# Kernel tuning notes

Measured on AMD Instinct MI355X. Metric: run time of the kernel, lower is better.

## Reference

```python
import jax, jax.numpy as jnp
import numpy as np

EPS = 1e-12

def _l2norm(x):
    # F.normalize(x, p=2, dim=1) applied on [B*N, D] == normalize last dim of [B, N, D]
    return x / jnp.maximum(jnp.linalg.norm(x, axis=-1, keepdims=True), EPS)

def setup_inputs() -> dict:
    key = jax.random.key(0)
    k1, k2 = jax.random.split(key)
    B, N, D = 128, 64, 128  # batch_size, num_epoch, feature_dim
    feat_k = jax.random.normal(k1, (B, N, D), dtype=jnp.float32)
    feat_q = jax.random.normal(k2, (B, N, D), dtype=jnp.float32)
    return {"feat_k": feat_k, "feat_q": feat_q}

def reference(feat_k, feat_q):
    B, N, D = feat_k.shape
    fk = _l2norm(feat_k)                       # [B, N, D]
    fq = jax.lax.stop_gradient(_l2norm(feat_q))  # sampler branch is no_grad

    # Dense pairwise similarities, as in the original einsum('ijk,mnk->ijnm')
    logits = jnp.einsum('ijk,mnk->ijnm', fk, fk)  # [B, N, N, B]
    sim    = jnp.einsum('ijk,mnk->ijnm', fq, fq)  # [B, N, N, B]

    el = jnp.exp(logits)

    # mask[i, j, n, m] = (m == i):
    #   pos[i, j] = sum_n exp(logits[i, j, n, i])
    pos = jnp.einsum('ijni->ij', el)              # diagonal over (i, m), summed over n

    #   neg[i, j] = sum_{n, m != i} exp(logits[i, j, n, m]) * sim[i, j, n, m]
    prod = el * sim
    neg = prod.sum(axis=(2, 3)) - jnp.einsum('ijni->ij', prod)

    loss = jnp.mean(-jnp.log(pos / (pos + neg)))
    return loss
```

## Files before the change

### kernel.cpp

```cpp
#include <hip/hip_runtime.h>
#include <stdint.h>

#define ROWS 8192
#define D    128
#define CSPLIT 16
#define CPS  (ROWS / CSPLIT)
#define BM   256
#define BN   64
#define NT   (CPS / BN)

typedef __bf16 bf16x8 __attribute__((ext_vector_type(8)));
typedef float  f32x4  __attribute__((ext_vector_type(4)));

typedef const __attribute__((address_space(1))) uint32_t guint;
typedef __attribute__((address_space(3))) uint32_t luint;

__device__ __forceinline__ void gload_lds16(const void* g, void* l) {
    __builtin_amdgcn_global_load_lds((guint*)g, (luint*)l, 16, 0, 0);
}

__device__ __forceinline__ ushort f2bf(float f) {
    union { float f; uint32_t u; } x; x.f = f;
    uint32_t r = x.u + 0x7FFFu + ((x.u >> 16) & 1u);
    return (ushort)(r >> 16);
}

__global__ __launch_bounds__(256) void k_norm(
    const float* __restrict__ fk, const float* __restrict__ fq,
    ushort* __restrict__ fkn, ushort* __restrict__ fqn)
{
    int gw = (blockIdx.x * 256 + threadIdx.x) >> 6;
    int l  = threadIdx.x & 63;
    const float* src; ushort* dst; int r;
    if (gw < ROWS) { src = fk; dst = fkn; r = gw; }
    else           { src = fq; dst = fqn; r = gw - ROWS; }
    float2 v = *reinterpret_cast<const float2*>(&src[r * D + l * 2]);
    float ss = v.x * v.x + v.y * v.y;
    #pragma unroll
    for (int m = 1; m < 64; m <<= 1) ss += __shfl_xor(ss, m, 64);
    float inv = 1.0f / fmaxf(sqrtf(ss), 1e-12f);
    ushort2 o; o.x = f2bf(v.x * inv); o.y = f2bf(v.y * inv);
    *reinterpret_cast<ushort2*>(&dst[r * D + l * 2]) = o;
}

__global__ __launch_bounds__(512, 4) void k_gram(
    const ushort* __restrict__ fkn, const ushort* __restrict__ fqn,
    float* __restrict__ pneg, float* __restrict__ ppos)
{
    __shared__ ushort lds[2][2 * BN * D];
    const int rt = blockIdx.x;
    const int cs = blockIdx.y;
    const int w  = threadIdx.x >> 6;
    const int l  = threadIdx.x & 63;
    const int lrow = l >> 4, lcol = l & 15;
    const int r0 = rt * BM;

    int off[2];
    #pragma unroll
    for (int i = 0; i < 2; ++i) {
        int L = w * 128 + i * 64 + l;
        int row = L >> 4, slot = L & 15;
        int col = slot ^ (row & 7);
        off[i] = row * 256 + col * 16;
    }

    bf16x8 ak[2][4], aq[2][4];
    #pragma unroll
    for (int rg = 0; rg < 2; ++rg) {
        int arow = r0 + w * 32 + rg * 16 + lcol;
        #pragma unroll
        for (int ks = 0; ks < 4; ++ks) {
            ak[rg][ks] = *reinterpret_cast<const bf16x8*>(fkn + arow * D + ks * 32 + lrow * 8);
            aq[rg][ks] = *reinterpret_cast<const bf16x8*>(fqn + arow * D + ks * 32 + lrow * 8);
        }
    }

    const int diagc = ((r0 + w * 32) >> 6) << 6;

    auto issue_stage = [&](int buf, int cbase) {
        const char* fkb = (const char*)fkn + (size_t)cbase * 256;
        const char* fqb = (const char*)fqn + (size_t)cbase * 256;
        ushort* lk = &lds[buf][w * 1024];
        ushort* lq = &lds[buf][BN * D + w * 1024];
        gload_lds16(fkb + off[0], lk);
        gload_lds16(fkb + off[1], lk + 512);
        gload_lds16(fqb + off[0], lq);
        gload_lds16(fqb + off[1], lq + 512);
    };

    float accp[2][4] = {{0.f,0.f,0.f,0.f},{0.f,0.f,0.f,0.f}};
    float accn[2][4] = {{0.f,0.f,0.f,0.f},{0.f,0.f,0.f,0.f}};

    issue_stage(0, cs * CPS);
    __syncthreads();

    int cur = 0;
    for (int t = 0; t < NT; ++t) {
        const int cbase = cs * CPS + t * BN;
        if (t + 1 < NT) issue_stage(cur ^ 1, cbase + BN);
        const bool diag = (cbase == diagc);
        const ushort* bkb = &lds[cur][0];
        const ushort* bqb = &lds[cur][BN * D];
        #pragma unroll
        for (int cc = 0; cc < 4; ++cc) {
            int brow = cc * 16 + lcol;
            f32x4 sk0 = {0,0,0,0}, sk1 = {0,0,0,0}, sq0 = {0,0,0,0}, sq1 = {0,0,0,0};
            #pragma unroll
            for (int ks = 0; ks < 4; ++ks) {
                int slot = (ks * 4 + lrow) ^ (brow & 7);
                bf16x8 bk = *reinterpret_cast<const bf16x8*>(bkb + brow * D + slot * 8);
                bf16x8 bq = *reinterpret_cast<const bf16x8*>(bqb + brow * D + slot * 8);
                sk0 = __builtin_amdgcn_mfma_f32_16x16x32_bf16(ak[0][ks], bk, sk0, 0, 0, 0);
                sk1 = __builtin_amdgcn_mfma_f32_16x16x32_bf16(ak[1][ks], bk, sk1, 0, 0, 0);
                sq0 = __builtin_amdgcn_mfma_f32_16x16x32_bf16(aq[0][ks], bq, sq0, 0, 0, 0);
                sq1 = __builtin_amdgcn_mfma_f32_16x16x32_bf16(aq[1][ks], bq, sq1, 0, 0, 0);
            }
            if (diag) {
                #pragma unroll
                for (int e = 0; e < 4; ++e) {
                    accp[0][e] += __expf(sk0[e]);
                    accp[1][e] += __expf(sk1[e]);
                }
            } else {
                #pragma unroll
                for (int e = 0; e < 4; ++e) {
                    accn[0][e] += __expf(sk0[e]) * sq0[e];
                    accn[1][e] += __expf(sk1[e]) * sq1[e];
                }
            }
        }
        __syncthreads();
        cur ^= 1;
    }

    #pragma unroll
    for (int m = 1; m <= 8; m <<= 1) {
        #pragma unroll
        for (int rg = 0; rg < 2; ++rg)
            #pragma unroll
            for (int e = 0; e < 4; ++e) {
                accp[rg][e] += __shfl_xor(accp[rg][e], m, 64);
                accn[rg][e] += __shfl_xor(accn[rg][e], m, 64);
            }
    }
    if (lcol == 0) {
        #pragma unroll
        for (int rg = 0; rg < 2; ++rg)
            #pragma unroll
            for (int e = 0; e < 4; ++e) {
                int gr = r0 + w * 32 + rg * 16 + lrow * 4 + e;
                ppos[cs * ROWS + gr] = accp[rg][e];
                pneg[cs * ROWS + gr] = accn[rg][e];
            }
    }
}

__global__ __launch_bounds__(256) void k_loss1(
    const float* __restrict__ pneg, const float* __restrict__ ppos,
    float* __restrict__ bsum)
{
    int r = blockIdx.x * 256 + threadIdx.x;
    float pos = 0.f, neg = 0.f;
    #pragma unroll
    for (int p = 0; p < CSPLIT; ++p) { pos += ppos[p * ROWS + r]; neg += pneg[p * ROWS + r]; }
    float s = log1pf(neg / pos);
    #pragma unroll
    for (int m = 1; m < 64; m <<= 1) s += __shfl_xor(s, m, 64);
    __shared__ float red[4];
    if ((threadIdx.x & 63) == 0) red[threadIdx.x >> 6] = s;
    __syncthreads();
    if (threadIdx.x == 0) bsum[blockIdx.x] = red[0] + red[1] + red[2] + red[3];
}

__global__ void k_loss2(const float* __restrict__ bsum, float* __restrict__ out)
{
    int l = threadIdx.x;
    float s = (l < 32) ? bsum[l] : 0.f;
    #pragma unroll
    for (int m = 1; m < 64; m <<= 1) s += __shfl_xor(s, m, 64);
    if (l == 0) out[0] = s * (1.0f / ROWS);
}

extern "C" void kernel_launch(void* const* d_in, const int* in_sizes, int n_in,
                              void* d_out, int out_size, void* d_ws, size_t ws_size,
                              hipStream_t stream)
{
    const float* fk = (const float*)d_in[0];
    const float* fq = (const float*)d_in[1];
    ushort* fkn = (ushort*)d_ws;
    ushort* fqn = fkn + ROWS * D;
    float*  pneg = (float*)(fqn + ROWS * D);
    float*  ppos = pneg + CSPLIT * ROWS;
    float*  bsum = ppos + CSPLIT * ROWS;

    k_norm<<<(2 * ROWS) / 4, 256, 0, stream>>>(fk, fq, fkn, fqn);
    k_gram<<<dim3(ROWS / BM, CSPLIT), 512, 0, stream>>>(fkn, fqn, pneg, ppos);
    k_loss1<<<32, 256, 0, stream>>>(pneg, ppos, bsum);
    k_loss2<<<1, 64, 0, stream>>>(bsum, (float*)d_out);
}
```

Measured before the change: 51.20 us.

## Use 4 waves with 64 rows each, fold log2e into k-normalization

Halves the gram block to 4 waves, each owning 64 A rows (4 row groups), so every B fragment read from LDS feeds four MFMAs instead of two. This cuts LDS read traffic per MFMA, at the cost of more registers and fewer resident waves. It also pre-scales the normalized k features by sqrt(log2 e), so the Gram entries are already in log2 units and a raw exp2 can replace __expf. The first tile's async load is issued before the A fragments are loaded, to overlap the two.

```diff
diff --git a/kernel.cpp b/kernel.cpp
--- a/kernel.cpp
+++ b/kernel.cpp
@@ -8,6 +8,7 @@
 #define BM   256
 #define BN   64
 #define NT   (CPS / BN)
+#define SQRT_LOG2E 1.2011224087864498f
 
 typedef __bf16 bf16x8 __attribute__((ext_vector_type(8)));
 typedef float  f32x4  __attribute__((ext_vector_type(4)));
@@ -31,19 +32,19 @@
 {
     int gw = (blockIdx.x * 256 + threadIdx.x) >> 6;
     int l  = threadIdx.x & 63;
-    const float* src; ushort* dst; int r;
-    if (gw < ROWS) { src = fk; dst = fkn; r = gw; }
-    else           { src = fq; dst = fqn; r = gw - ROWS; }
+    const float* src; ushort* dst; int r; float scale;
+    if (gw < ROWS) { src = fk; dst = fkn; r = gw; scale = SQRT_LOG2E; }
+    else           { src = fq; dst = fqn; r = gw - ROWS; scale = 1.0f; }
     float2 v = *reinterpret_cast<const float2*>(&src[r * D + l * 2]);
     float ss = v.x * v.x + v.y * v.y;
     #pragma unroll
     for (int m = 1; m < 64; m <<= 1) ss += __shfl_xor(ss, m, 64);
-    float inv = 1.0f / fmaxf(sqrtf(ss), 1e-12f);
+    float inv = scale / fmaxf(sqrtf(ss), 1e-12f);
     ushort2 o; o.x = f2bf(v.x * inv); o.y = f2bf(v.y * inv);
     *reinterpret_cast<ushort2*>(&dst[r * D + l * 2]) = o;
 }
 
-__global__ __launch_bounds__(512, 4) void k_gram(
+__global__ __launch_bounds__(256, 2) void k_gram(
     const ushort* __restrict__ fkn, const ushort* __restrict__ fqn,
     float* __restrict__ pneg, float* __restrict__ ppos)
 {
@@ -55,19 +56,31 @@
     const int lrow = l >> 4, lcol = l & 15;
     const int r0 = rt * BM;
 
-    int off[2];
-    #pragma unroll
-    for (int i = 0; i < 2; ++i) {
-        int L = w * 128 + i * 64 + l;
+    int off[4];
+    #pragma unroll
+    for (int t = 0; t < 4; ++t) {
+        int L = t * 256 + w * 64 + l;
         int row = L >> 4, slot = L & 15;
         int col = slot ^ (row & 7);
-        off[i] = row * 256 + col * 16;
-    }
-
-    bf16x8 ak[2][4], aq[2][4];
-    #pragma unroll
-    for (int rg = 0; rg < 2; ++rg) {
-        int arow = r0 + w * 32 + rg * 16 + lcol;
+        off[t] = row * 256 + col * 16;
+    }
+
+    auto issue_stage = [&](int buf, int cbase) {
+        const char* fkb = (const char*)fkn + (size_t)cbase * 256;
+        const char* fqb = (const char*)fqn + (size_t)cbase * 256;
+        #pragma unroll
+        for (int t = 0; t < 4; ++t) {
+            gload_lds16(fkb + off[t], &lds[buf][t * 2048 + w * 512]);
+            gload_lds16(fqb + off[t], &lds[buf][BN * D + t * 2048 + w * 512]);
+        }
+    };
+
+    issue_stage(0, cs * CPS);
+
+    bf16x8 ak[4][4], aq[4][4];
+    #pragma unroll
+    for (int rg = 0; rg < 4; ++rg) {
+        int arow = r0 + w * 64 + rg * 16 + lcol;
         #pragma unroll
         for (int ks = 0; ks < 4; ++ks) {
             ak[rg][ks] = *reinterpret_cast<const bf16x8*>(fkn + arow * D + ks * 32 + lrow * 8);
@@ -75,23 +88,11 @@
         }
     }
 
-    const int diagc = ((r0 + w * 32) >> 6) << 6;
-
-    auto issue_stage = [&](int buf, int cbase) {
-        const char* fkb = (const char*)fkn + (size_t)cbase * 256;
-        const char* fqb = (const char*)fqn + (size_t)cbase * 256;
-        ushort* lk = &lds[buf][w * 1024];
-        ushort* lq = &lds[buf][BN * D + w * 1024];
-        gload_lds16(fkb + off[0], lk);
-        gload_lds16(fkb + off[1], lk + 512);
-        gload_lds16(fqb + off[0], lq);
-        gload_lds16(fqb + off[1], lq + 512);
-    };
-
-    float accp[2][4] = {{0.f,0.f,0.f,0.f},{0.f,0.f,0.f,0.f}};
-    float accn[2][4] = {{0.f,0.f,0.f,0.f},{0.f,0.f,0.f,0.f}};
-
-    issue_stage(0, cs * CPS);
+    const int diagc = r0 + w * 64;
+
+    float accp[4][4] = {};
+    float accn[4][4] = {};
+
     __syncthreads();
 
     int cur = 0;
@@ -104,29 +105,31 @@
         #pragma unroll
         for (int cc = 0; cc < 4; ++cc) {
             int brow = cc * 16 + lcol;
-            f32x4 sk0 = {0,0,0,0}, sk1 = {0,0,0,0}, sq0 = {0,0,0,0}, sq1 = {0,0,0,0};
+            f32x4 sk[4] = {{0,0,0,0},{0,0,0,0},{0,0,0,0},{0,0,0,0}};
+            f32x4 sq[4] = {{0,0,0,0},{0,0,0,0},{0,0,0,0},{0,0,0,0}};
             #pragma unroll
             for (int ks = 0; ks < 4; ++ks) {
                 int slot = (ks * 4 + lrow) ^ (brow & 7);
                 bf16x8 bk = *reinterpret_cast<const bf16x8*>(bkb + brow * D + slot * 8);
                 bf16x8 bq = *reinterpret_cast<const bf16x8*>(bqb + brow * D + slot * 8);
-                sk0 = __builtin_amdgcn_mfma_f32_16x16x32_bf16(ak[0][ks], bk, sk0, 0, 0, 0);
-                sk1 = __builtin_amdgcn_mfma_f32_16x16x32_bf16(ak[1][ks], bk, sk1, 0, 0, 0);
-                sq0 = __builtin_amdgcn_mfma_f32_16x16x32_bf16(aq[0][ks], bq, sq0, 0, 0, 0);
-                sq1 = __builtin_amdgcn_mfma_f32_16x16x32_bf16(aq[1][ks], bq, sq1, 0, 0, 0);
+                #pragma unroll
+                for (int rg = 0; rg < 4; ++rg) {
+                    sk[rg] = __builtin_amdgcn_mfma_f32_16x16x32_bf16(ak[rg][ks], bk, sk[rg], 0, 0, 0);
+                    sq[rg] = __builtin_amdgcn_mfma_f32_16x16x32_bf16(aq[rg][ks], bq, sq[rg], 0, 0, 0);
+                }
             }
             if (diag) {
                 #pragma unroll
-                for (int e = 0; e < 4; ++e) {
-                    accp[0][e] += __expf(sk0[e]);
-                    accp[1][e] += __expf(sk1[e]);
-                }
+                for (int rg = 0; rg < 4; ++rg)
+                    #pragma unroll
+                    for (int e = 0; e < 4; ++e)
+                        accp[rg][e] += __builtin_exp2f(sk[rg][e]);
             } else {
                 #pragma unroll
-                for (int e = 0; e < 4; ++e) {
-                    accn[0][e] += __expf(sk0[e]) * sq0[e];
-                    accn[1][e] += __expf(sk1[e]) * sq1[e];
-                }
+                for (int rg = 0; rg < 4; ++rg)
+                    #pragma unroll
+                    for (int e = 0; e < 4; ++e)
+                        accn[rg][e] += __builtin_exp2f(sk[rg][e]) * sq[rg][e];
             }
         }
         __syncthreads();
@@ -136,7 +139,7 @@
     #pragma unroll
     for (int m = 1; m <= 8; m <<= 1) {
         #pragma unroll
-        for (int rg = 0; rg < 2; ++rg)
+        for (int rg = 0; rg < 4; ++rg)
             #pragma unroll
             for (int e = 0; e < 4; ++e) {
                 accp[rg][e] += __shfl_xor(accp[rg][e], m, 64);
@@ -145,10 +148,10 @@
     }
     if (lcol == 0) {
         #pragma unroll
-        for (int rg = 0; rg < 2; ++rg)
+        for (int rg = 0; rg < 4; ++rg)
             #pragma unroll
             for (int e = 0; e < 4; ++e) {
-                int gr = r0 + w * 32 + rg * 16 + lrow * 4 + e;
+                int gr = r0 + w * 64 + rg * 16 + lrow * 4 + e;
                 ppos[cs * ROWS + gr] = accp[rg][e];
                 pneg[cs * ROWS + gr] = accn[rg][e];
             }
@@ -194,7 +197,7 @@
     float*  bsum = ppos + CSPLIT * ROWS;
 
     k_norm<<<(2 * ROWS) / 4, 256, 0, stream>>>(fk, fq, fkn, fqn);
-    k_gram<<<dim3(ROWS / BM, CSPLIT), 512, 0, stream>>>(fkn, fqn, pneg, ppos);
+    k_gram<<<dim3(ROWS / BM, CSPLIT), 256, 0, stream>>>(fkn, fqn, pneg, ppos);
     k_loss1<<<32, 256, 0, stream>>>(pneg, ppos, bsum);
     k_loss2<<<1, 64, 0, stream>>>(bsum, (float*)d_out);
 }
```

Measured after the change: 55.90 us. +9.2%, slower.

## Deepen LDS pipeline to four stages and fold log2e into normalization

Applied to the files above, without the earlier changes.

Reworks the gram kernel's staging from a double buffer of 64-column tiles to a four-deep ring of 32-column tiles. Three stages are prefetched up front and the loop waits with a manual vmcnt wait and a single barrier. The k vectors are prescaled by sqrt(log2 e) so exp2 can replace expf, B fragments are loaded before the MFMA chain, and setprio is raised around the MFMAs. The aim is to hide global-to-LDS latency and trim exp cost, at the price of more barriers per column and some fragile hand-written wait counts.

```diff
diff --git a/kernel.cpp b/kernel.cpp
--- a/kernel.cpp
+++ b/kernel.cpp
@@ -6,8 +6,9 @@
 #define CSPLIT 16
 #define CPS  (ROWS / CSPLIT)
 #define BM   256
-#define BN   64
+#define BN   32
 #define NT   (CPS / BN)
+#define SQRT_LOG2E 1.2011224087864498f
 
 typedef __bf16 bf16x8 __attribute__((ext_vector_type(8)));
 typedef float  f32x4  __attribute__((ext_vector_type(4)));
@@ -31,14 +32,14 @@
 {
     int gw = (blockIdx.x * 256 + threadIdx.x) >> 6;
     int l  = threadIdx.x & 63;
-    const float* src; ushort* dst; int r;
-    if (gw < ROWS) { src = fk; dst = fkn; r = gw; }
-    else           { src = fq; dst = fqn; r = gw - ROWS; }
+    const float* src; ushort* dst; int r; float scale;
+    if (gw < ROWS) { src = fk; dst = fkn; r = gw; scale = SQRT_LOG2E; }
+    else           { src = fq; dst = fqn; r = gw - ROWS; scale = 1.0f; }
     float2 v = *reinterpret_cast<const float2*>(&src[r * D + l * 2]);
     float ss = v.x * v.x + v.y * v.y;
     #pragma unroll
     for (int m = 1; m < 64; m <<= 1) ss += __shfl_xor(ss, m, 64);
-    float inv = 1.0f / fmaxf(sqrtf(ss), 1e-12f);
+    float inv = scale / fmaxf(sqrtf(ss), 1e-12f);
     ushort2 o; o.x = f2bf(v.x * inv); o.y = f2bf(v.y * inv);
     *reinterpret_cast<ushort2*>(&dst[r * D + l * 2]) = o;
 }
@@ -47,7 +48,7 @@
     const ushort* __restrict__ fkn, const ushort* __restrict__ fqn,
     float* __restrict__ pneg, float* __restrict__ ppos)
 {
-    __shared__ ushort lds[2][2 * BN * D];
+    __shared__ ushort lds[4][2][BN][128];
     const int rt = blockIdx.x;
     const int cs = blockIdx.y;
     const int w  = threadIdx.x >> 6;
@@ -55,14 +56,22 @@
     const int lrow = l >> 4, lcol = l & 15;
     const int r0 = rt * BM;
 
-    int off[2];
-    #pragma unroll
-    for (int i = 0; i < 2; ++i) {
-        int L = w * 128 + i * 64 + l;
+    int soff;
+    {
+        int L = threadIdx.x;
         int row = L >> 4, slot = L & 15;
-        int col = slot ^ (row & 7);
-        off[i] = row * 256 + col * 16;
-    }
+        soff = row * 256 + (slot ^ (row & 7)) * 16;
+    }
+
+    auto issue_stage = [&](int buf, int cbase) {
+        gload_lds16((const char*)fkn + (size_t)cbase * 256 + soff, &lds[buf][0][0][0] + (size_t)threadIdx.x * 8);
+        gload_lds16((const char*)fqn + (size_t)cbase * 256 + soff, &lds[buf][1][0][0] + (size_t)threadIdx.x * 8);
+    };
+
+    const int cbase0 = cs * CPS;
+    issue_stage(0, cbase0);
+    issue_stage(1, cbase0 + BN);
+    issue_stage(2, cbase0 + 2 * BN);
 
     bf16x8 ak[2][4], aq[2][4];
     #pragma unroll
@@ -75,62 +84,54 @@
         }
     }
 
-    const int diagc = ((r0 + w * 32) >> 6) << 6;
-
-    auto issue_stage = [&](int buf, int cbase) {
-        const char* fkb = (const char*)fkn + (size_t)cbase * 256;
-        const char* fqb = (const char*)fqn + (size_t)cbase * 256;
-        ushort* lk = &lds[buf][w * 1024];
-        ushort* lq = &lds[buf][BN * D + w * 1024];
-        gload_lds16(fkb + off[0], lk);
-        gload_lds16(fkb + off[1], lk + 512);
-        gload_lds16(fqb + off[0], lq);
-        gload_lds16(fqb + off[1], lq + 512);
-    };
-
-    float accp[2][4] = {{0.f,0.f,0.f,0.f},{0.f,0.f,0.f,0.f}};
-    float accn[2][4] = {{0.f,0.f,0.f,0.f},{0.f,0.f,0.f,0.f}};
-
-    issue_stage(0, cs * CPS);
-    __syncthreads();
-
-    int cur = 0;
+    const int diagc = (r0 + w * 32) & ~63;
+
+    float accp[2][4] = {};
+    float accn[2][4] = {};
+
     for (int t = 0; t < NT; ++t) {
-        const int cbase = cs * CPS + t * BN;
-        if (t + 1 < NT) issue_stage(cur ^ 1, cbase + BN);
-        const bool diag = (cbase == diagc);
-        const ushort* bkb = &lds[cur][0];
-        const ushort* bqb = &lds[cur][BN * D];
-        #pragma unroll
-        for (int cc = 0; cc < 4; ++cc) {
+        asm volatile("s_waitcnt vmcnt(4)" ::: "memory");
+        __builtin_amdgcn_s_barrier();
+        if (t + 3 < NT) issue_stage((t + 3) & 3, cbase0 + (t + 3) * BN);
+
+        const int cbase = cbase0 + t * BN;
+        const bool diag = ((cbase & ~63) == diagc);
+        const ushort* bkb = &lds[t & 3][0][0][0];
+        const ushort* bqb = &lds[t & 3][1][0][0];
+        #pragma unroll
+        for (int cc = 0; cc < 2; ++cc) {
             int brow = cc * 16 + lcol;
-            f32x4 sk0 = {0,0,0,0}, sk1 = {0,0,0,0}, sq0 = {0,0,0,0}, sq1 = {0,0,0,0};
+            bf16x8 bk[4], bq[4];
             #pragma unroll
             for (int ks = 0; ks < 4; ++ks) {
                 int slot = (ks * 4 + lrow) ^ (brow & 7);
-                bf16x8 bk = *reinterpret_cast<const bf16x8*>(bkb + brow * D + slot * 8);
-                bf16x8 bq = *reinterpret_cast<const bf16x8*>(bqb + brow * D + slot * 8);
-                sk0 = __builtin_amdgcn_mfma_f32_16x16x32_bf16(ak[0][ks], bk, sk0, 0, 0, 0);
-                sk1 = __builtin_amdgcn_mfma_f32_16x16x32_bf16(ak[1][ks], bk, sk1, 0, 0, 0);
-                sq0 = __builtin_amdgcn_mfma_f32_16x16x32_bf16(aq[0][ks], bq, sq0, 0, 0, 0);
-                sq1 = __builtin_amdgcn_mfma_f32_16x16x32_bf16(aq[1][ks], bq, sq1, 0, 0, 0);
-            }
+                bk[ks] = *reinterpret_cast<const bf16x8*>(bkb + brow * 128 + slot * 8);
+                bq[ks] = *reinterpret_cast<const bf16x8*>(bqb + brow * 128 + slot * 8);
+            }
+            f32x4 sk0 = {0,0,0,0}, sk1 = {0,0,0,0}, sq0 = {0,0,0,0}, sq1 = {0,0,0,0};
+            __builtin_amdgcn_s_setprio(1);
+            #pragma unroll
+            for (int ks = 0; ks < 4; ++ks) {
+                sk0 = __builtin_amdgcn_mfma_f32_16x16x32_bf16(ak[0][ks], bk[ks], sk0, 0, 0, 0);
+                sk1 = __builtin_amdgcn_mfma_f32_16x16x32_bf16(ak[1][ks], bk[ks], sk1, 0, 0, 0);
+                sq0 = __builtin_amdgcn_mfma_f32_16x16x32_bf16(aq[0][ks], bq[ks], sq0, 0, 0, 0);
+                sq1 = __builtin_amdgcn_mfma_f32_16x16x32_bf16(aq[1][ks], bq[ks], sq1, 0, 0, 0);
+            }
+            __builtin_amdgcn_s_setprio(0);
             if (diag) {
                 #pragma unroll
                 for (int e = 0; e < 4; ++e) {
-                    accp[0][e] += __expf(sk0[e]);
-                    accp[1][e] += __expf(sk1[e]);
+                    accp[0][e] += __builtin_exp2f(sk0[e]);
+                    accp[1][e] += __builtin_exp2f(sk1[e]);
                 }
             } else {
                 #pragma unroll
                 for (int e = 0; e < 4; ++e) {
-                    accn[0][e] += __expf(sk0[e]) * sq0[e];
-                    accn[1][e] += __expf(sk1[e]) * sq1[e];
+                    accn[0][e] += __builtin_exp2f(sk0[e]) * sq0[e];
+                    accn[1][e] += __builtin_exp2f(sk1[e]) * sq1[e];
                 }
             }
         }
-        __syncthreads();
-        cur ^= 1;
     }
 
     #pragma unroll
```

Result: slower. 66.58 us (+30.0%).
